# Optimization experiments

Measured on AMD Instinct MI355X. Metric: run time of the kernel, lower is better.

The kernel has to match this reference:

```python
import jax, jax.numpy as jnp
import numpy as np

VOCAB = 100000
EMB = 20
HID = 10
SEQ = 100
NLAB = 15
BATCH = 16384


def setup_inputs() -> dict:
    key = jax.random.key(0)
    ks = jax.random.split(key, 7)
    x = jax.random.randint(ks[0], (BATCH, SEQ), 0, VOCAB, dtype=jnp.int32)
    embed_table = jax.random.normal(ks[1], (VOCAB, EMB), dtype=jnp.float32) * 0.05
    # Keras LSTMCell kernels: input kernel [EMB, 4H], recurrent kernel [HID, 4H], bias [4H]
    Wx = jax.random.normal(ks[2], (EMB, 4 * HID), dtype=jnp.float32) * (1.0 / np.sqrt(EMB))
    Wh = jax.random.normal(ks[3], (HID, 4 * HID), dtype=jnp.float32) * (1.0 / np.sqrt(HID))
    b = jnp.zeros((4 * HID,), dtype=jnp.float32).at[HID:2 * HID].set(1.0)  # unit forget bias
    Wd = jax.random.normal(ks[4], (HID, NLAB), dtype=jnp.float32) * (1.0 / np.sqrt(HID))
    bd = jnp.zeros((NLAB,), dtype=jnp.float32)
    return {"x": x, "embed_table": embed_table, "Wx": Wx, "Wh": Wh, "b": b,
            "Wd": Wd, "bd": bd, "drop_rate": 0}


def _lstm(e, Wx, Wh, b):
    # e: [B, T, E]. Precompute input projections for all steps at once.
    zx = jnp.einsum('bte,eg->btg', e, Wx) + b  # [B, T, 4H]
    B = e.shape[0]
    h0 = jnp.zeros((B, HID), dtype=e.dtype)
    c0 = jnp.zeros((B, HID), dtype=e.dtype)

    def step(carry, zx_t):
        h, c = carry
        z = zx_t + h @ Wh  # [B, 4H]
        zi, zf, zc, zo = jnp.split(z, 4, axis=-1)  # Keras gate order i,f,c,o
        i = jax.nn.sigmoid(zi)
        f = jax.nn.sigmoid(zf)
        o = jax.nn.sigmoid(zo)
        c_new = f * c + i * jnp.tanh(zc)
        h_new = o * jnp.tanh(c_new)
        return (h_new, c_new), None

    (hT, _), _ = jax.lax.scan(step, (h0, c0), jnp.swapaxes(zx, 0, 1))  # scan over time
    return hT  # [B, H]


def reference(x, embed_table, Wx, Wh, b, Wd, bd, drop_rate):
    e = embed_table[x]  # [B, T, E] embedding lookup
    h = _lstm(e, Wx, Wh, b)  # final hidden state, [B, H]
    # tf.nn.dropout with rate == drop_rate == 0 is an identity
    logits = h @ Wd + bd  # [B, NLAB]
    return logits
```

## Files before the change

### kernel.cpp

```cpp
#include <hip/hip_runtime.h>
#include <hip/hip_fp16.h>

#define VOCAB 100000
#define EMB   20
#define HID   10
#define SEQ   100
#define NLAB  15
#define BATCH 16384
#define GATES 40
#define PROWH 48

__device__ __forceinline__ float exp2_f(float x){ float r; asm("v_exp_f32 %0, %1" : "=v"(r) : "v"(x)); return r; }
__device__ __forceinline__ float rcp_f(float x){ float r; asm("v_rcp_f32 %0, %1" : "=v"(r) : "v"(x)); return r; }

__device__ __host__ __forceinline__ constexpr float gscale(int G){
  return (G == 2) ? -2.885390081777927f : -1.442695040888963f;
}

template<int CTRL>
__device__ __forceinline__ float qb(float x){
  return __int_as_float(__builtin_amdgcn_mov_dpp(__float_as_int(x), CTRL, 0xF, 0xF, true));
}

__global__ __launch_bounds__(256)
void proj_kernel(const float* __restrict__ emb, const float* __restrict__ Wx,
                 const float* __restrict__ bias, __half* __restrict__ P)
{
  __shared__ float Wxl[EMB * PROWH];
  __shared__ float bl[PROWH];
  const int tid = threadIdx.x;
  for (int i = tid; i < EMB * PROWH; i += 256) {
    int k = i / PROWH, slot = i - k * PROWH;
    int sb = slot / 12, r = slot - sb * 12, G = r / 3, s = r - G * 3, u = s * 4 + sb;
    Wxl[i] = (u < HID) ? Wx[k * GATES + G * HID + u] * gscale(G) : 0.f;
  }
  if (tid < PROWH) {
    int slot = tid, sb = slot / 12, r = slot - sb * 12, G = r / 3, s = r - G * 3, u = s * 4 + sb;
    bl[slot] = (u < HID) ? bias[G * HID + u] * gscale(G) : 0.f;
  }
  __syncthreads();

  const int v   = blockIdx.x * 64 + (tid >> 2);
  const int sub = tid & 3;
  if (v >= VOCAB) return;

  const float4* er = (const float4*)(emb + (size_t)v * EMB);
  float4 e0 = er[0], e1 = er[1], e2 = er[2], e3 = er[3], e4 = er[4];
  float e[EMB] = {e0.x,e0.y,e0.z,e0.w, e1.x,e1.y,e1.z,e1.w, e2.x,e2.y,e2.z,e2.w,
                  e3.x,e3.y,e3.z,e3.w, e4.x,e4.y,e4.z,e4.w};
  const int wb = sub * 12;
  float acc[12];
  #pragma unroll
  for (int j = 0; j < 12; ++j) acc[j] = bl[wb + j];
  #pragma unroll
  for (int k = 0; k < EMB; ++k)
    #pragma unroll
    for (int j = 0; j < 12; ++j)
      acc[j] = fmaf(e[k], Wxl[k * PROWH + wb + j], acc[j]);

  union { __half h[12]; int2 i2[3]; } u;
  #pragma unroll
  for (int j = 0; j < 12; ++j) u.h[j] = __float2half(acc[j]);
  int2* o = (int2*)(P + (size_t)v * PROWH + wb);
  o[0] = u.i2[0]; o[1] = u.i2[1]; o[2] = u.i2[2];
}

__device__ __forceinline__ void cvt12(const int2 b[3], float z[12]) {
  #pragma unroll
  for (int q = 0; q < 3; ++q) {
    float2 f0 = __half22float2(*(const __half2*)&b[q].x);
    float2 f1 = __half22float2(*(const __half2*)&b[q].y);
    z[q*4+0] = f0.x; z[q*4+1] = f0.y; z[q*4+2] = f1.x; z[q*4+3] = f1.y;
  }
}

template<bool USEP>
__global__ __launch_bounds__(256, 1)
void rnn_kernel(const int* __restrict__ x, const __half* __restrict__ P,
                const float* __restrict__ Wh, const float* __restrict__ Wd,
                const float* __restrict__ bd, float* __restrict__ out,
                const float* __restrict__ emb, const float* __restrict__ Wx,
                const float* __restrict__ bias)
{
  __shared__ int   xs[64 * SEQ];
  __shared__ float Wxl[EMB * PROWH];
  __shared__ float bls[PROWH];

  const int tid = threadIdx.x;
  const int lb  = tid >> 2;
  const int sub = tid & 3;
  const int b0  = blockIdx.x * 64;

  for (int i = tid; i < 64 * SEQ; i += 256) xs[i] = x[(size_t)b0 * SEQ + i];

  if constexpr (!USEP) {
    for (int i = tid; i < EMB * PROWH; i += 256) {
      int k = i / PROWH, slot = i - k * PROWH;
      int sb2 = slot / 12, r = slot - sb2 * 12, G = r / 3, s = r - G * 3, u = s * 4 + sb2;
      Wxl[i] = (u < HID) ? Wx[k * GATES + G * HID + u] * gscale(G) : 0.f;
    }
    if (tid < PROWH) {
      int slot = tid, sb2 = slot / 12, r = slot - sb2 * 12, G = r / 3, s = r - G * 3, u = s * 4 + sb2;
      bls[slot] = (u < HID) ? bias[G * HID + u] * gscale(G) : 0.f;
    }
  }

  float Whr[HID][12];
  #pragma unroll
  for (int j = 0; j < 12; ++j) {
    const int G = j / 3, s = j - G * 3, u = s * 4 + sub;
    #pragma unroll
    for (int k = 0; k < HID; ++k)
      Whr[k][j] = (u < HID) ? Wh[k * GATES + G * HID + u] * gscale(G) : 0.f;
  }

  __syncthreads();

  float h[HID], cst[3];
  #pragma unroll
  for (int k = 0; k < HID; ++k) h[k] = 0.f;
  cst[0] = cst[1] = cst[2] = 0.f;

  const int* xrow = xs + lb * SEQ;

  if constexpr (USEP) {
    int2 pA[3], pB[3], pC[3];
    auto ldrow = [&](int2 (&p)[3], int t) {
      int row = xrow[t < SEQ ? t : SEQ - 1];
      const int2* q = (const int2*)(P + (size_t)row * PROWH + sub * 12);
      p[0] = q[0]; p[1] = q[1]; p[2] = q[2];
    };
    ldrow(pA, 0); ldrow(pB, 1); ldrow(pC, 2);

    auto lstm_step = [&](int2 (&p)[3], int t) {
      float z[12];
      cvt12(p, z);
      ldrow(p, t + 3);

      #pragma unroll
      for (int k = 0; k < HID; ++k)
        #pragma unroll
        for (int j = 0; j < 12; ++j)
          z[j] = fmaf(h[k], Whr[k][j], z[j]);

      float a[12];
      #pragma unroll
      for (int j = 0; j < 12; ++j) {
        float r = rcp_f(1.f + exp2_f(z[j]));
        a[j] = (j / 3 == 2) ? fmaf(2.f, r, -1.f) : r;
      }

      float hl[3];
      #pragma unroll
      for (int s = 0; s < 3; ++s) {
        cst[s] = fmaf(a[3 + s], cst[s], a[s] * a[6 + s]);
        float r = rcp_f(1.f + exp2_f(-2.885390081777927f * cst[s]));
        hl[s] = fmaf(a[9 + s], r + r, -a[9 + s]);
      }

      h[0] = qb<0x00>(hl[0]); h[1] = qb<0x55>(hl[0]); h[2] = qb<0xAA>(hl[0]); h[3] = qb<0xFF>(hl[0]);
      h[4] = qb<0x00>(hl[1]); h[5] = qb<0x55>(hl[1]); h[6] = qb<0xAA>(hl[1]); h[7] = qb<0xFF>(hl[1]);
      h[8] = qb<0x00>(hl[2]); h[9] = qb<0x55>(hl[2]);
    };

    #pragma unroll 1
    for (int t = 0; t < SEQ - 1; t += 3) {
      lstm_step(pA, t);
      lstm_step(pB, t + 1);
      lstm_step(pC, t + 2);
    }
    lstm_step(pA, SEQ - 1);
  } else {
    float bb[12];
    #pragma unroll
    for (int j = 0; j < 12; ++j) bb[j] = bls[sub * 12 + j];
    float4 e0, e1, e2, e3, e4;
    {
      int row = xrow[0];
      const float4* q = (const float4*)(emb + (size_t)row * EMB);
      e0 = q[0]; e1 = q[1]; e2 = q[2]; e3 = q[3]; e4 = q[4];
    }
    #pragma unroll 1
    for (int t = 0; t < SEQ; ++t) {
      float e[EMB] = {e0.x,e0.y,e0.z,e0.w, e1.x,e1.y,e1.z,e1.w, e2.x,e2.y,e2.z,e2.w,
                      e3.x,e3.y,e3.z,e3.w, e4.x,e4.y,e4.z,e4.w};
      float z[12];
      #pragma unroll
      for (int j = 0; j < 12; ++j) z[j] = bb[j];
      const int wbase = sub * 12;
      #pragma unroll
      for (int k = 0; k < EMB; ++k)
        #pragma unroll
        for (int j = 0; j < 12; ++j)
          z[j] = fmaf(e[k], Wxl[k * PROWH + wbase + j], z[j]);
      if (t + 1 < SEQ) {
        int row = xrow[t + 1];
        const float4* q = (const float4*)(emb + (size_t)row * EMB);
        e0 = q[0]; e1 = q[1]; e2 = q[2]; e3 = q[3]; e4 = q[4];
      }
      #pragma unroll
      for (int k = 0; k < HID; ++k)
        #pragma unroll
        for (int j = 0; j < 12; ++j)
          z[j] = fmaf(h[k], Whr[k][j], z[j]);
      float a[12];
      #pragma unroll
      for (int j = 0; j < 12; ++j) {
        float r = rcp_f(1.f + exp2_f(z[j]));
        a[j] = (j / 3 == 2) ? fmaf(2.f, r, -1.f) : r;
      }
      float hl[3];
      #pragma unroll
      for (int s = 0; s < 3; ++s) {
        cst[s] = fmaf(a[3 + s], cst[s], a[s] * a[6 + s]);
        float r = rcp_f(1.f + exp2_f(-2.885390081777927f * cst[s]));
        hl[s] = fmaf(a[9 + s], r + r, -a[9 + s]);
      }
      h[0] = qb<0x00>(hl[0]); h[1] = qb<0x55>(hl[0]); h[2] = qb<0xAA>(hl[0]); h[3] = qb<0xFF>(hl[0]);
      h[4] = qb<0x00>(hl[1]); h[5] = qb<0x55>(hl[1]); h[6] = qb<0xAA>(hl[1]); h[7] = qb<0xFF>(hl[1]);
      h[8] = qb<0x00>(hl[2]); h[9] = qb<0x55>(hl[2]);
    }
  }

  #pragma unroll
  for (int s = 0; s < 4; ++s) {
    int j = s * 4 + sub;
    if (j < NLAB) {
      float acc = bd[j];
      #pragma unroll
      for (int k = 0; k < HID; ++k)
        acc = fmaf(h[k], Wd[k * NLAB + j], acc);
      out[(size_t)(b0 + lb) * NLAB + j] = acc;
    }
  }
}

extern "C" void kernel_launch(void* const* d_in, const int* in_sizes, int n_in,
                              void* d_out, int out_size, void* d_ws, size_t ws_size,
                              hipStream_t stream) {
  (void)in_sizes; (void)n_in; (void)out_size;
  const int*   x    = (const int*)  d_in[0];
  const float* emb  = (const float*)d_in[1];
  const float* Wx   = (const float*)d_in[2];
  const float* Wh   = (const float*)d_in[3];
  const float* bias = (const float*)d_in[4];
  const float* Wd   = (const float*)d_in[5];
  const float* bd   = (const float*)d_in[6];
  float* out = (float*)d_out;

  const size_t pbytes = (size_t)VOCAB * PROWH * sizeof(__half);
  if (ws_size >= pbytes) {
    __half* P = (__half*)d_ws;
    hipLaunchKernelGGL(proj_kernel, dim3((VOCAB + 63) / 64), dim3(256), 0, stream,
                       emb, Wx, bias, P);
    hipLaunchKernelGGL((rnn_kernel<true>), dim3(BATCH / 64), dim3(256), 0, stream,
                       x, P, Wh, Wd, bd, out, emb, Wx, bias);
  } else {
    hipLaunchKernelGGL((rnn_kernel<false>), dim3(BATCH / 64), dim3(256), 0, stream,
                       x, (const __half*)nullptr, Wh, Wd, bd, out, emb, Wx, bias);
  }
}
```

Measured before the change: 66.50 us.

## Use packed fp16 dot2 for recurrent matvec and merge gate reciprocals

The recurrent h·Wh product now uses fp16 packed pairs with v_dot2 (fdot2) instead of 120 fp32 FMAs per step. Wh is stored as half2 registers, and h is broadcast across the quad as packed halves via DPP. Gate activations are restructured so sigmoid(i)*tanh(c) and sigmoid(o)*tanh(cell) each share one reciprocal, which cuts the transcendental count. The cost is lower precision in the hidden-state recurrence, with error that can accumulate over 100 steps.

```diff
diff --git a/kernel.cpp b/kernel.cpp
--- a/kernel.cpp
+++ b/kernel.cpp
@@ -10,6 +10,8 @@
 #define GATES 40
 #define PROWH 48
 
+typedef _Float16 half2_t __attribute__((ext_vector_type(2)));
+
 __device__ __forceinline__ float exp2_f(float x){ float r; asm("v_exp_f32 %0, %1" : "=v"(r) : "v"(x)); return r; }
 __device__ __forceinline__ float rcp_f(float x){ float r; asm("v_rcp_f32 %0, %1" : "=v"(r) : "v"(x)); return r; }
 
@@ -20,6 +22,20 @@
 template<int CTRL>
 __device__ __forceinline__ float qb(float x){
   return __int_as_float(__builtin_amdgcn_mov_dpp(__float_as_int(x), CTRL, 0xF, 0xF, true));
+}
+template<int CTRL>
+__device__ __forceinline__ int qbi(int x){
+  return __builtin_amdgcn_mov_dpp(x, CTRL, 0xF, 0xF, true);
+}
+
+__device__ __forceinline__ half2_t h2cast(int i){ union{int i; half2_t h;} u; u.i=i; return u.h; }
+
+__device__ __forceinline__ float fdot2(half2_t a, half2_t b, float c){
+#if __has_builtin(__builtin_amdgcn_fdot2)
+  return __builtin_amdgcn_fdot2(a, b, c, false);
+#else
+  return fmaf((float)a[1], (float)b[1], fmaf((float)a[0], (float)b[0], c));
+#endif
 }
 
 __global__ __launch_bounds__(256)
@@ -105,25 +121,37 @@
     }
   }
 
-  float Whr[HID][12];
-  #pragma unroll
-  for (int j = 0; j < 12; ++j) {
-    const int G = j / 3, s = j - G * 3, u = s * 4 + sub;
-    #pragma unroll
-    for (int k = 0; k < HID; ++k)
-      Whr[k][j] = (u < HID) ? Wh[k * GATES + G * HID + u] * gscale(G) : 0.f;
-  }
-
   __syncthreads();
 
-  float h[HID], cst[3];
-  #pragma unroll
-  for (int k = 0; k < HID; ++k) h[k] = 0.f;
+  float cst[3];
   cst[0] = cst[1] = cst[2] = 0.f;
 
   const int* xrow = xs + lb * SEQ;
 
   if constexpr (USEP) {
+    half2_t w2[5][12];
+    #pragma unroll
+    for (int p = 0; p < 5; ++p) {
+      const int k0 = (p < 4) ? p : 8;
+      const int k1 = (p < 4) ? p + 4 : 9;
+      #pragma unroll
+      for (int j = 0; j < 12; ++j) {
+        const int G = j / 3, s = j - G * 3, u = s * 4 + sub;
+        float a = 0.f, b2 = 0.f;
+        if (u < HID) {
+          a  = Wh[k0 * GATES + G * HID + u] * gscale(G);
+          b2 = Wh[k1 * GATES + G * HID + u] * gscale(G);
+        }
+        w2[p][j][0] = (_Float16)a;
+        w2[p][j][1] = (_Float16)b2;
+      }
+    }
+
+    int hpi[5] = {0, 0, 0, 0, 0};
+    float hf[HID];
+    #pragma unroll
+    for (int k = 0; k < HID; ++k) hf[k] = 0.f;
+
     int2 pA[3], pB[3], pC[3];
     auto ldrow = [&](int2 (&p)[3], int t) {
       int row = xrow[t < SEQ ? t : SEQ - 1];
@@ -138,29 +166,38 @@
       ldrow(p, t + 3);
 
       #pragma unroll
-      for (int k = 0; k < HID; ++k)
+      for (int pp = 0; pp < 5; ++pp) {
+        half2_t hp = h2cast(hpi[pp]);
         #pragma unroll
         for (int j = 0; j < 12; ++j)
-          z[j] = fmaf(h[k], Whr[k][j], z[j]);
-
-      float a[12];
-      #pragma unroll
-      for (int j = 0; j < 12; ++j) {
-        float r = rcp_f(1.f + exp2_f(z[j]));
-        a[j] = (j / 3 == 2) ? fmaf(2.f, r, -1.f) : r;
+          z[j] = fdot2(hp, w2[pp][j], z[j]);
       }
 
       float hl[3];
       #pragma unroll
       for (int s = 0; s < 3; ++s) {
-        cst[s] = fmaf(a[3 + s], cst[s], a[s] * a[6 + s]);
-        float r = rcp_f(1.f + exp2_f(-2.885390081777927f * cst[s]));
-        hl[s] = fmaf(a[9 + s], r + r, -a[9 + s]);
-      }
-
-      h[0] = qb<0x00>(hl[0]); h[1] = qb<0x55>(hl[0]); h[2] = qb<0xAA>(hl[0]); h[3] = qb<0xFF>(hl[0]);
-      h[4] = qb<0x00>(hl[1]); h[5] = qb<0x55>(hl[1]); h[6] = qb<0xAA>(hl[1]); h[7] = qb<0xFF>(hl[1]);
-      h[8] = qb<0x00>(hl[2]); h[9] = qb<0x55>(hl[2]);
+        float Ei = exp2_f(z[s]);
+        float Ef = exp2_f(z[s + 3]);
+        float Ec = exp2_f(z[s + 6]);
+        float Eo = exp2_f(z[s + 9]);
+        float f  = rcp_f(1.f + Ef);
+        float ig = (1.f - Ec) * rcp_f((1.f + Ei) * (1.f + Ec));
+        cst[s] = fmaf(f, cst[s], ig);
+        float Et = exp2_f(-2.885390081777927f * cst[s]);
+        hl[s] = (1.f - Et) * rcp_f((1.f + Eo) * (1.f + Et));
+      }
+
+      hf[0] = hl[0]; hf[1] = hl[1]; hf[2] = hl[2];
+
+      union { _Float16 h[2]; int i; } u01, u2;
+      u01.h[0] = (_Float16)hl[0]; u01.h[1] = (_Float16)hl[1];
+      u2.h[0]  = (_Float16)hl[2]; u2.h[1]  = (_Float16)0.f;
+      hpi[0] = qbi<0x00>(u01.i);
+      hpi[1] = qbi<0x55>(u01.i);
+      hpi[2] = qbi<0xAA>(u01.i);
+      hpi[3] = qbi<0xFF>(u01.i);
+      hpi[4] = (int)__builtin_amdgcn_perm((unsigned)qbi<0x55>(u2.i),
+                                          (unsigned)qbi<0x00>(u2.i), 0x05040100u);
     };
 
     #pragma unroll 1
@@ -170,7 +207,35 @@
       lstm_step(pC, t + 2);
     }
     lstm_step(pA, SEQ - 1);
+
+    float h[HID];
+    h[0] = qb<0x00>(hf[0]); h[1] = qb<0x55>(hf[0]); h[2] = qb<0xAA>(hf[0]); h[3] = qb<0xFF>(hf[0]);
+    h[4] = qb<0x00>(hf[1]); h[5] = qb<0x55>(hf[1]); h[6] = qb<0xAA>(hf[1]); h[7] = qb<0xFF>(hf[1]);
+    h[8] = qb<0x00>(hf[2]); h[9] = qb<0x55>(hf[2]);
+
+    #pragma unroll
+    for (int s = 0; s < 4; ++s) {
+      int j = s * 4 + sub;
+      if (j < NLAB) {
+        float acc = bd[j];
+        #pragma unroll
+        for (int k = 0; k < HID; ++k)
+          acc = fmaf(h[k], Wd[k * NLAB + j], acc);
+        out[(size_t)(b0 + lb) * NLAB + j] = acc;
+      }
+    }
   } else {
+    float Whr[HID][12];
+    #pragma unroll
+    for (int j = 0; j < 12; ++j) {
+      const int G = j / 3, s = j - G * 3, u = s * 4 + sub;
+      #pragma unroll
+      for (int k = 0; k < HID; ++k)
+        Whr[k][j] = (u < HID) ? Wh[k * GATES + G * HID + u] * gscale(G) : 0.f;
+    }
+    float h[HID];
+    #pragma unroll
+    for (int k = 0; k < HID; ++k) h[k] = 0.f;
     float bb[12];
     #pragma unroll
     for (int j = 0; j < 12; ++j) bb[j] = bls[sub * 12 + j];
@@ -203,34 +268,30 @@
         #pragma unroll
         for (int j = 0; j < 12; ++j)
           z[j] = fmaf(h[k], Whr[k][j], z[j]);
-      float a[12];
-      #pragma unroll
-      for (int j = 0; j < 12; ++j) {
-        float r = rcp_f(1.f + exp2_f(z[j]));
-        a[j] = (j / 3 == 2) ? fmaf(2.f, r, -1.f) : r;
-      }
       float hl[3];
       #pragma unroll
       for (int s = 0; s < 3; ++s) {
-        cst[s] = fmaf(a[3 + s], cst[s], a[s] * a[6 + s]);
-        float r = rcp_f(1.f + exp2_f(-2.885390081777927f * cst[s]));
-        hl[s] = fmaf(a[9 + s], r + r, -a[9 + s]);
+        float Ei = exp2_f(z[s]), Ef = exp2_f(z[s+3]), Ec = exp2_f(z[s+6]), Eo = exp2_f(z[s+9]);
+        float f  = rcp_f(1.f + Ef);
+        float ig = (1.f - Ec) * rcp_f((1.f + Ei) * (1.f + Ec));
+        cst[s] = fmaf(f, cst[s], ig);
+        float Et = exp2_f(-2.885390081777927f * cst[s]);
+        hl[s] = (1.f - Et) * rcp_f((1.f + Eo) * (1.f + Et));
       }
       h[0] = qb<0x00>(hl[0]); h[1] = qb<0x55>(hl[0]); h[2] = qb<0xAA>(hl[0]); h[3] = qb<0xFF>(hl[0]);
       h[4] = qb<0x00>(hl[1]); h[5] = qb<0x55>(hl[1]); h[6] = qb<0xAA>(hl[1]); h[7] = qb<0xFF>(hl[1]);
       h[8] = qb<0x00>(hl[2]); h[9] = qb<0x55>(hl[2]);
     }
-  }
-
-  #pragma unroll
-  for (int s = 0; s < 4; ++s) {
-    int j = s * 4 + sub;
-    if (j < NLAB) {
-      float acc = bd[j];
-      #pragma unroll
-      for (int k = 0; k < HID; ++k)
-        acc = fmaf(h[k], Wd[k * NLAB + j], acc);
-      out[(size_t)(b0 + lb) * NLAB + j] = acc;
+    #pragma unroll
+    for (int s = 0; s < 4; ++s) {
+      int j = s * 4 + sub;
+      if (j < NLAB) {
+        float acc = bd[j];
+        #pragma unroll
+        for (int k = 0; k < HID; ++k)
+          acc = fmaf(h[k], Wd[k * NLAB + j], acc);
+        out[(size_t)(b0 + lb) * NLAB + j] = acc;
+      }
     }
   }
 }
```

Result: faster. 57.27 us (-13.9%).
